# Performance work log

Hardware: AMD Instinct MI355X
Metric: run time of the kernel (lower is better)

The kernel has to match this reference:

```python
import jax, jax.numpy as jnp
import numpy as np

DEPTH_VALID_MIN = 1e-4   # cfg.depth_valid_min
IOU_THRESH = 0.02        # cfg.collision_iou_thresh
TOPK = 64                # cfg.collision_topk


def setup_inputs() -> dict:
    key = jax.random.key(0)
    k1, k2, k3, k4 = jax.random.split(key, 4)
    N, H, W = 128, 512, 512
    boxes = jax.random.uniform(k1, (N, 4), dtype=jnp.float32)
    masks = jax.random.uniform(k2, (N, H, W), dtype=jnp.float32)
    conf = jax.random.uniform(k3, (N,), dtype=jnp.float32)
    depth = jax.random.uniform(k4, (H, W), dtype=jnp.float32)
    return {"boxes": boxes, "masks": masks, "conf": conf, "depth": depth}


def _mask_depth_var(depth, mask):
    # population variance of depth pixels where mask>0.5 and depth>valid_min
    valid = (mask > 0.5) & (depth > DEPTH_VALID_MIN)
    cnt = jnp.sum(valid)
    cntf = jnp.maximum(cnt, 1).astype(depth.dtype)
    mean = jnp.sum(jnp.where(valid, depth, 0.0)) / cntf
    var = jnp.sum(jnp.where(valid, (depth - mean) ** 2, 0.0)) / cntf
    return jnp.where(cnt > 0, var, 0.0)


def reference(boxes, masks, conf, depth):
    N = boxes.shape[0]
    x1, y1, x2, y2 = boxes[:, 0], boxes[:, 1], boxes[:, 2], boxes[:, 3]
    bw = jnp.maximum(x2 - x1, 0.0)
    bh = jnp.maximum(y2 - y1, 0.0)
    area = jnp.clip(bw * bh, 0.0, 1.0)

    # per-detection masked depth variance (vectorized over N)
    d_var = jax.vmap(lambda m: _mask_depth_var(depth, m))(masks)  # [N]

    tall = jnp.clip(bh / (bw + 1e-6), 0.0, 10.0)
    thinness = jax.nn.sigmoid((tall - 1.2) * 2.0)
    unstable = jnp.clip(0.35 * thinness + 0.35 * jax.nn.sigmoid(d_var * 6.0)
                        + 0.3 * (1.0 - conf), 0.0, 1.0)
    slip = jnp.clip(0.45 * jax.nn.sigmoid(d_var * 8.0) + 0.25 * (1.0 - conf)
                    + 0.3 * jax.nn.sigmoid((area - 0.05) * 3.0), 0.0, 1.0)
    support = jnp.clip(1.0 - unstable, 0.0, 1.0)

    # pairwise IoU [N,N]
    xx1 = jnp.maximum(x1[:, None], x1[None, :])
    yy1 = jnp.maximum(y1[:, None], y1[None, :])
    xx2 = jnp.minimum(x2[:, None], x2[None, :])
    yy2 = jnp.minimum(y2[:, None], y2[None, :])
    inter = jnp.maximum(xx2 - xx1, 0.0) * jnp.maximum(yy2 - yy1, 0.0)
    a = bw * bh
    union = a[:, None] + a[None, :] - inter
    iou = inter / (union + 1e-6)
    iou = iou * (1.0 - jnp.eye(N, dtype=iou.dtype))  # fill_diagonal_(0)

    # collision pairs: top-k over off-diagonal IoUs above threshold (padded to TOPK)
    flat = iou.ravel()
    masked = jnp.where(flat > IOU_THRESH, flat, -1.0)
    vals, idx = jax.lax.top_k(masked, TOPK)
    valid = vals > IOU_THRESH
    pairs = jnp.where(valid[:, None],
                      jnp.stack([idx // N, idx % N], axis=-1), 0).astype(jnp.int32)
    collision = jnp.where(valid, jnp.clip(vals * 5.0, 0.0, 1.0), 0.0)

    return unstable, slip, support, pairs, collision
```

## Files before the change

### kernel.cpp

```cpp
#include <hip/hip_runtime.h>
#include <stdint.h>

#define N_BOX 128
#define HW    262144
#define SPLIT 16
#define CHUNK (HW / SPLIT)
#define TOPK  64
typedef unsigned long long u64;

__global__ __launch_bounds__(256) void k_mask_partial(
    const float* __restrict__ masks, const float* __restrict__ depth,
    float* __restrict__ part) {
  const int b = blockIdx.x;
  const int m = b >> 4;
  const int s = b & (SPLIT - 1);
  const float4* mk = reinterpret_cast<const float4*>(masks + (size_t)m * HW + (size_t)s * CHUNK);
  const float4* dp = reinterpret_cast<const float4*>(depth + (size_t)s * CHUNK);
  const int t = threadIdx.x;

  float c = 0.f, s1 = 0.f, s2 = 0.f;
#pragma unroll
  for (int j = 0; j < 16; ++j) {
    const int i = t + j * 256;
    float4 mv = mk[i];
    float4 dv = dp[i];
    if (mv.x > 0.5f && dv.x > 1e-4f) { c += 1.f; s1 += dv.x; s2 += dv.x * dv.x; }
    if (mv.y > 0.5f && dv.y > 1e-4f) { c += 1.f; s1 += dv.y; s2 += dv.y * dv.y; }
    if (mv.z > 0.5f && dv.z > 1e-4f) { c += 1.f; s1 += dv.z; s2 += dv.z * dv.z; }
    if (mv.w > 0.5f && dv.w > 1e-4f) { c += 1.f; s1 += dv.w; s2 += dv.w * dv.w; }
  }
  for (int off = 32; off > 0; off >>= 1) {
    c  += __shfl_down(c,  off);
    s1 += __shfl_down(s1, off);
    s2 += __shfl_down(s2, off);
  }
  __shared__ float red[3][4];
  const int wid = t >> 6, lane = t & 63;
  if (lane == 0) { red[0][wid] = c; red[1][wid] = s1; red[2][wid] = s2; }
  __syncthreads();
  if (t == 0) {
    part[b * 3 + 0] = red[0][0] + red[0][1] + red[0][2] + red[0][3];
    part[b * 3 + 1] = red[1][0] + red[1][1] + red[1][2] + red[1][3];
    part[b * 3 + 2] = red[2][0] + red[2][1] + red[2][2] + red[2][3];
  }
}

__device__ __forceinline__ u64 sort64_desc(u64 v, int lane) {
#pragma unroll
  for (int size = 2; size <= 64; size <<= 1) {
#pragma unroll
    for (int stride = size >> 1; stride > 0; stride >>= 1) {
      const u64 o = __shfl_xor(v, stride);
      const bool blk   = ((lane & size) == 0);
      const bool lower = ((lane & stride) == 0);
      const u64 mx = (v > o) ? v : o;
      const u64 mn = (v > o) ? o : v;
      v = (blk == lower) ? mx : mn;
    }
  }
  return v;
}

__device__ __forceinline__ u64 merge64_desc(u64 v, u64 s, int lane) {
  const u64 r = __shfl_xor(s, 63);
  v = (v > r) ? v : r;
#pragma unroll
  for (int stride = 32; stride > 0; stride >>= 1) {
    const u64 o = __shfl_xor(v, stride);
    const bool lower = ((lane & stride) == 0);
    const u64 mx = (v > o) ? v : o;
    const u64 mn = (v > o) ? o : v;
    v = lower ? mx : mn;
  }
  return v;
}

__device__ __forceinline__ float sigf(float x) { return 1.f / (1.f + expf(-x)); }

__global__ __launch_bounds__(1024) void k_topk_fin(
    const float* __restrict__ boxes, const float* __restrict__ conf,
    const float* __restrict__ part, float* __restrict__ out) {
  __shared__ float X1[N_BOX], Y1[N_BOX], X2[N_BOX], Y2[N_BOX], A[N_BOX];
  __shared__ u64 wtop[16][TOPK];

  const int t = threadIdx.x;
  const int lane = t & 63;
  const int w = t >> 6;

  if (t < N_BOX) {
    const float x1 = boxes[t * 4 + 0], y1 = boxes[t * 4 + 1];
    const float x2 = boxes[t * 4 + 2], y2 = boxes[t * 4 + 3];
    X1[t] = x1; Y1[t] = y1; X2[t] = x2; Y2[t] = y2;
    A[t] = fmaxf(x2 - x1, 0.f) * fmaxf(y2 - y1, 0.f);
  }
  __syncthreads();

  u64 v = 0ULL;
#pragma unroll
  for (int b = 0; b < 16; ++b) {
    const int e = w * 1024 + b * 64 + lane;
    const int i = e >> 7, jj = e & 127;
    const float xx1 = fmaxf(X1[i], X1[jj]);
    const float yy1 = fmaxf(Y1[i], Y1[jj]);
    const float xx2 = fminf(X2[i], X2[jj]);
    const float yy2 = fminf(Y2[i], Y2[jj]);
    const float inter = fmaxf(xx2 - xx1, 0.f) * fmaxf(yy2 - yy1, 0.f);
    const float uni = A[i] + A[jj] - inter;
    float iou = inter / (uni + 1e-6f);
    if (i == jj) iou = 0.f;
    const float mval = (iou > 0.02f) ? iou : -1.0f;
    uint32_t u = __float_as_uint(mval);
    u = (u & 0x80000000u) ? ~u : (u | 0x80000000u);
    const u64 key = ((u64)u << 32) | (u64)(0xFFFFFFFFu - (uint32_t)e);

    if (b == 0) {
      v = sort64_desc(key, lane);
    } else {
      const u64 cut = __shfl(v, 63);
      if (__any(key > cut)) {
        const u64 s = sort64_desc(key, lane);
        v = merge64_desc(v, s, lane);
      }
    }
  }
  wtop[w][lane] = v;
  __syncthreads();

  if (w == 0) {
#pragma unroll
    for (int ww = 1; ww < 16; ++ww)
      v = merge64_desc(v, wtop[ww][lane], lane);
    const uint32_t mh = (uint32_t)(v >> 32);
    const uint32_t u  = (mh & 0x80000000u) ? (mh ^ 0x80000000u) : ~mh;
    const float val   = __uint_as_float(u);
    const uint32_t e  = 0xFFFFFFFFu - (uint32_t)(v & 0xFFFFFFFFu);
    const bool valid  = (val > 0.02f);
    out[3 * N_BOX + 2 * lane + 0] = valid ? (float)(e >> 7)  : 0.f;
    out[3 * N_BOX + 2 * lane + 1] = valid ? (float)(e & 127) : 0.f;
    out[3 * N_BOX + 2 * TOPK + lane] = valid ? fminf(fmaxf(val * 5.f, 0.f), 1.f) : 0.f;
  } else if (w == 2 || w == 3) {
    const int m = t - 128;
    float C = 0.f, S1 = 0.f, S2 = 0.f;
#pragma unroll
    for (int s = 0; s < SPLIT; ++s) {
      C  += part[(m * SPLIT + s) * 3 + 0];
      S1 += part[(m * SPLIT + s) * 3 + 1];
      S2 += part[(m * SPLIT + s) * 3 + 2];
    }
    const float cntf = fmaxf(C, 1.f);
    const float mean = S1 / cntf;
    float var = S2 / cntf - mean * mean;
    var = (C > 0.f) ? fmaxf(var, 0.f) : 0.f;

    const float x1 = X1[m], y1 = Y1[m], x2 = X2[m], y2 = Y2[m];
    const float bw = fmaxf(x2 - x1, 0.f);
    const float bh = fmaxf(y2 - y1, 0.f);
    const float area = fminf(fmaxf(bw * bh, 0.f), 1.f);
    const float cf = conf[m];
    const float tall = fminf(fmaxf(bh / (bw + 1e-6f), 0.f), 10.f);
    const float thin = sigf((tall - 1.2f) * 2.f);
    const float unst = fminf(fmaxf(0.35f * thin + 0.35f * sigf(var * 6.f) + 0.3f * (1.f - cf), 0.f), 1.f);
    const float slip = fminf(fmaxf(0.45f * sigf(var * 8.f) + 0.25f * (1.f - cf) + 0.3f * sigf((area - 0.05f) * 3.f), 0.f), 1.f);
    out[m]             = unst;
    out[N_BOX + m]     = slip;
    out[2 * N_BOX + m] = fminf(fmaxf(1.f - unst, 0.f), 1.f);
  }
}

extern "C" void kernel_launch(void* const* d_in, const int* in_sizes, int n_in,
                              void* d_out, int out_size, void* d_ws, size_t ws_size,
                              hipStream_t stream) {
  const float* boxes = (const float*)d_in[0];
  const float* masks = (const float*)d_in[1];
  const float* conf  = (const float*)d_in[2];
  const float* depth = (const float*)d_in[3];
  float* out  = (float*)d_out;
  float* part = (float*)d_ws;

  hipLaunchKernelGGL(k_mask_partial, dim3(N_BOX * SPLIT), dim3(256), 0, stream,
                     masks, depth, part);
  hipLaunchKernelGGL(k_topk_fin, dim3(1), dim3(1024), 0, stream,
                     boxes, conf, part, out);
}
```

Measured before the change: 218.3 us.

## Fuse mask reduction and top-k into one kernel with last-block finalize

```diff
diff --git a/kernel.cpp b/kernel.cpp
--- a/kernel.cpp
+++ b/kernel.cpp
@@ -6,44 +6,9 @@
 #define SPLIT 16
 #define CHUNK (HW / SPLIT)
 #define TOPK  64
+#define NMASKBLK (N_BOX * SPLIT)
 typedef unsigned long long u64;
-
-__global__ __launch_bounds__(256) void k_mask_partial(
-    const float* __restrict__ masks, const float* __restrict__ depth,
-    float* __restrict__ part) {
-  const int b = blockIdx.x;
-  const int m = b >> 4;
-  const int s = b & (SPLIT - 1);
-  const float4* mk = reinterpret_cast<const float4*>(masks + (size_t)m * HW + (size_t)s * CHUNK);
-  const float4* dp = reinterpret_cast<const float4*>(depth + (size_t)s * CHUNK);
-  const int t = threadIdx.x;
-
-  float c = 0.f, s1 = 0.f, s2 = 0.f;
-#pragma unroll
-  for (int j = 0; j < 16; ++j) {
-    const int i = t + j * 256;
-    float4 mv = mk[i];
-    float4 dv = dp[i];
-    if (mv.x > 0.5f && dv.x > 1e-4f) { c += 1.f; s1 += dv.x; s2 += dv.x * dv.x; }
-    if (mv.y > 0.5f && dv.y > 1e-4f) { c += 1.f; s1 += dv.y; s2 += dv.y * dv.y; }
-    if (mv.z > 0.5f && dv.z > 1e-4f) { c += 1.f; s1 += dv.z; s2 += dv.z * dv.z; }
-    if (mv.w > 0.5f && dv.w > 1e-4f) { c += 1.f; s1 += dv.w; s2 += dv.w * dv.w; }
-  }
-  for (int off = 32; off > 0; off >>= 1) {
-    c  += __shfl_down(c,  off);
-    s1 += __shfl_down(s1, off);
-    s2 += __shfl_down(s2, off);
-  }
-  __shared__ float red[3][4];
-  const int wid = t >> 6, lane = t & 63;
-  if (lane == 0) { red[0][wid] = c; red[1][wid] = s1; red[2][wid] = s2; }
-  __syncthreads();
-  if (t == 0) {
-    part[b * 3 + 0] = red[0][0] + red[0][1] + red[0][2] + red[0][3];
-    part[b * 3 + 1] = red[1][0] + red[1][1] + red[1][2] + red[1][3];
-    part[b * 3 + 2] = red[2][0] + red[2][1] + red[2][2] + red[2][3];
-  }
-}
+typedef float vf4 __attribute__((ext_vector_type(4)));
 
 __device__ __forceinline__ u64 sort64_desc(u64 v, int lane) {
 #pragma unroll
@@ -77,93 +42,141 @@
 
 __device__ __forceinline__ float sigf(float x) { return 1.f / (1.f + expf(-x)); }
 
-__global__ __launch_bounds__(1024) void k_topk_fin(
-    const float* __restrict__ boxes, const float* __restrict__ conf,
-    const float* __restrict__ part, float* __restrict__ out) {
-  __shared__ float X1[N_BOX], Y1[N_BOX], X2[N_BOX], Y2[N_BOX], A[N_BOX];
-  __shared__ u64 wtop[16][TOPK];
-
+__global__ __launch_bounds__(1024) void k_fused(
+    const float* __restrict__ boxes, const float* __restrict__ masks,
+    const float* __restrict__ conf, const float* __restrict__ depth,
+    float* __restrict__ part, unsigned* __restrict__ cnt,
+    float* __restrict__ out) {
   const int t = threadIdx.x;
   const int lane = t & 63;
   const int w = t >> 6;
 
-  if (t < N_BOX) {
-    const float x1 = boxes[t * 4 + 0], y1 = boxes[t * 4 + 1];
-    const float x2 = boxes[t * 4 + 2], y2 = boxes[t * 4 + 3];
-    X1[t] = x1; Y1[t] = y1; X2[t] = x2; Y2[t] = y2;
-    A[t] = fmaxf(x2 - x1, 0.f) * fmaxf(y2 - y1, 0.f);
-  }
-  __syncthreads();
+  __shared__ float red[3][16];
+  __shared__ int   isLast;
+  __shared__ float X1[N_BOX], Y1[N_BOX], X2[N_BOX], Y2[N_BOX], A[N_BOX];
+  __shared__ u64   wtop[16][TOPK];
 
-  u64 v = 0ULL;
+  if (blockIdx.x < NMASKBLK) {
+    const int b = blockIdx.x;
+    const int m = b >> 4;
+    const int s = b & (SPLIT - 1);
+    const vf4* mk = reinterpret_cast<const vf4*>(masks + (size_t)m * HW + (size_t)s * CHUNK);
+    const vf4* dp = reinterpret_cast<const vf4*>(depth + (size_t)s * CHUNK);
+
+    float c = 0.f, s1 = 0.f, s2 = 0.f;
 #pragma unroll
-  for (int b = 0; b < 16; ++b) {
-    const int e = w * 1024 + b * 64 + lane;
-    const int i = e >> 7, jj = e & 127;
-    const float xx1 = fmaxf(X1[i], X1[jj]);
-    const float yy1 = fmaxf(Y1[i], Y1[jj]);
-    const float xx2 = fminf(X2[i], X2[jj]);
-    const float yy2 = fminf(Y2[i], Y2[jj]);
-    const float inter = fmaxf(xx2 - xx1, 0.f) * fmaxf(yy2 - yy1, 0.f);
-    const float uni = A[i] + A[jj] - inter;
-    float iou = inter / (uni + 1e-6f);
-    if (i == jj) iou = 0.f;
-    const float mval = (iou > 0.02f) ? iou : -1.0f;
-    uint32_t u = __float_as_uint(mval);
-    u = (u & 0x80000000u) ? ~u : (u | 0x80000000u);
-    const u64 key = ((u64)u << 32) | (u64)(0xFFFFFFFFu - (uint32_t)e);
+    for (int j = 0; j < 4; ++j) {
+      const int i = t + j * 1024;
+      const vf4 mv = __builtin_nontemporal_load(&mk[i]);
+      const vf4 dv = dp[i];
+      if (mv.x > 0.5f && dv.x > 1e-4f) { c += 1.f; s1 += dv.x; s2 += dv.x * dv.x; }
+      if (mv.y > 0.5f && dv.y > 1e-4f) { c += 1.f; s1 += dv.y; s2 += dv.y * dv.y; }
+      if (mv.z > 0.5f && dv.z > 1e-4f) { c += 1.f; s1 += dv.z; s2 += dv.z * dv.z; }
+      if (mv.w > 0.5f && dv.w > 1e-4f) { c += 1.f; s1 += dv.w; s2 += dv.w * dv.w; }
+    }
+    for (int off = 32; off > 0; off >>= 1) {
+      c  += __shfl_down(c,  off);
+      s1 += __shfl_down(s1, off);
+      s2 += __shfl_down(s2, off);
+    }
+    if (lane == 0) { red[0][w] = c; red[1][w] = s1; red[2][w] = s2; }
+    __syncthreads();
+    if (t == 0) {
+      float C = 0.f, S1 = 0.f, S2 = 0.f;
+#pragma unroll
+      for (int k = 0; k < 16; ++k) { C += red[0][k]; S1 += red[1][k]; S2 += red[2][k]; }
+      part[b * 3 + 0] = C;
+      part[b * 3 + 1] = S1;
+      part[b * 3 + 2] = S2;
+      __threadfence();
+      const unsigned tk = atomicAdd(cnt, 1u);
+      isLast = (tk == NMASKBLK - 1) ? 1 : 0;
+    }
+    __syncthreads();
 
-    if (b == 0) {
-      v = sort64_desc(key, lane);
-    } else {
-      const u64 cut = __shfl(v, 63);
-      if (__any(key > cut)) {
-        const u64 s = sort64_desc(key, lane);
-        v = merge64_desc(v, s, lane);
+    if (isLast && t < N_BOX) {
+      __threadfence();
+      volatile const float* vp = part;
+      const int m2 = t;
+      float C = 0.f, S1 = 0.f, S2 = 0.f;
+#pragma unroll
+      for (int s2i = 0; s2i < SPLIT; ++s2i) {
+        C  += vp[(m2 * SPLIT + s2i) * 3 + 0];
+        S1 += vp[(m2 * SPLIT + s2i) * 3 + 1];
+        S2 += vp[(m2 * SPLIT + s2i) * 3 + 2];
+      }
+      const float cntf = fmaxf(C, 1.f);
+      const float mean = S1 / cntf;
+      float var = S2 / cntf - mean * mean;
+      var = (C > 0.f) ? fmaxf(var, 0.f) : 0.f;
+
+      const float x1 = boxes[m2 * 4 + 0], y1 = boxes[m2 * 4 + 1];
+      const float x2 = boxes[m2 * 4 + 2], y2 = boxes[m2 * 4 + 3];
+      const float bw = fmaxf(x2 - x1, 0.f);
+      const float bh = fmaxf(y2 - y1, 0.f);
+      const float area = fminf(fmaxf(bw * bh, 0.f), 1.f);
+      const float cf = conf[m2];
+      const float tall = fminf(fmaxf(bh / (bw + 1e-6f), 0.f), 10.f);
+      const float thin = sigf((tall - 1.2f) * 2.f);
+      const float unst = fminf(fmaxf(0.35f * thin + 0.35f * sigf(var * 6.f) + 0.3f * (1.f - cf), 0.f), 1.f);
+      const float slip = fminf(fmaxf(0.45f * sigf(var * 8.f) + 0.25f * (1.f - cf) + 0.3f * sigf((area - 0.05f) * 3.f), 0.f), 1.f);
+      out[m2]             = unst;
+      out[N_BOX + m2]     = slip;
+      out[2 * N_BOX + m2] = fminf(fmaxf(1.f - unst, 0.f), 1.f);
+    }
+  } else {
+    if (t < N_BOX) {
+      const float x1 = boxes[t * 4 + 0], y1 = boxes[t * 4 + 1];
+      const float x2 = boxes[t * 4 + 2], y2 = boxes[t * 4 + 3];
+      X1[t] = x1; Y1[t] = y1; X2[t] = x2; Y2[t] = y2;
+      A[t] = fmaxf(x2 - x1, 0.f) * fmaxf(y2 - y1, 0.f);
+    }
+    __syncthreads();
+
+    u64 v = 0ULL;
+#pragma unroll
+    for (int b = 0; b < 16; ++b) {
+      const int e = w * 1024 + b * 64 + lane;
+      const int i = e >> 7, jj = e & 127;
+      const float xx1 = fmaxf(X1[i], X1[jj]);
+      const float yy1 = fmaxf(Y1[i], Y1[jj]);
+      const float xx2 = fminf(X2[i], X2[jj]);
+      const float yy2 = fminf(Y2[i], Y2[jj]);
+      const float inter = fmaxf(xx2 - xx1, 0.f) * fmaxf(yy2 - yy1, 0.f);
+      const float uni = A[i] + A[jj] - inter;
+      float iou = inter / (uni + 1e-6f);
+      if (i == jj) iou = 0.f;
+      const float mval = (iou > 0.02f) ? iou : -1.0f;
+      uint32_t u = __float_as_uint(mval);
+      u = (u & 0x80000000u) ? ~u : (u | 0x80000000u);
+      const u64 key = ((u64)u << 32) | (u64)(0xFFFFFFFFu - (uint32_t)e);
+
+      if (b == 0) {
+        v = sort64_desc(key, lane);
+      } else {
+        const u64 cut = __shfl(v, 63);
+        if (__any(key > cut)) {
+          const u64 s = sort64_desc(key, lane);
+          v = merge64_desc(v, s, lane);
+        }
       }
     }
-  }
-  wtop[w][lane] = v;
-  __syncthreads();
+    wtop[w][lane] = v;
+    __syncthreads();
 
-  if (w == 0) {
+    if (w == 0) {
 #pragma unroll
-    for (int ww = 1; ww < 16; ++ww)
-      v = merge64_desc(v, wtop[ww][lane], lane);
-    const uint32_t mh = (uint32_t)(v >> 32);
-    const uint32_t u  = (mh & 0x80000000u) ? (mh ^ 0x80000000u) : ~mh;
-    const float val   = __uint_as_float(u);
-    const uint32_t e  = 0xFFFFFFFFu - (uint32_t)(v & 0xFFFFFFFFu);
-    const bool valid  = (val > 0.02f);
-    out[3 * N_BOX + 2 * lane + 0] = valid ? (float)(e >> 7)  : 0.f;
-    out[3 * N_BOX + 2 * lane + 1] = valid ? (float)(e & 127) : 0.f;
-    out[3 * N_BOX + 2 * TOPK + lane] = valid ? fminf(fmaxf(val * 5.f, 0.f), 1.f) : 0.f;
-  } else if (w == 2 || w == 3) {
-    const int m = t - 128;
-    float C = 0.f, S1 = 0.f, S2 = 0.f;
-#pragma unroll
-    for (int s = 0; s < SPLIT; ++s) {
-      C  += part[(m * SPLIT + s) * 3 + 0];
-      S1 += part[(m * SPLIT + s) * 3 + 1];
-      S2 += part[(m * SPLIT + s) * 3 + 2];
+      for (int ww = 1; ww < 16; ++ww)
+        v = merge64_desc(v, wtop[ww][lane], lane);
+      const uint32_t mh = (uint32_t)(v >> 32);
+      const uint32_t u  = (mh & 0x80000000u) ? (mh ^ 0x80000000u) : ~mh;
+      const float val   = __uint_as_float(u);
+      const uint32_t e  = 0xFFFFFFFFu - (uint32_t)(v & 0xFFFFFFFFu);
+      const bool valid  = (val > 0.02f);
+      out[3 * N_BOX + 2 * lane + 0] = valid ? (float)(e >> 7)  : 0.f;
+      out[3 * N_BOX + 2 * lane + 1] = valid ? (float)(e & 127) : 0.f;
+      out[3 * N_BOX + 2 * TOPK + lane] = valid ? fminf(fmaxf(val * 5.f, 0.f), 1.f) : 0.f;
     }
-    const float cntf = fmaxf(C, 1.f);
-    const float mean = S1 / cntf;
-    float var = S2 / cntf - mean * mean;
-    var = (C > 0.f) ? fmaxf(var, 0.f) : 0.f;
-
-    const float x1 = X1[m], y1 = Y1[m], x2 = X2[m], y2 = Y2[m];
-    const float bw = fmaxf(x2 - x1, 0.f);
-    const float bh = fmaxf(y2 - y1, 0.f);
-    const float area = fminf(fmaxf(bw * bh, 0.f), 1.f);
-    const float cf = conf[m];
-    const float tall = fminf(fmaxf(bh / (bw + 1e-6f), 0.f), 10.f);
-    const float thin = sigf((tall - 1.2f) * 2.f);
-    const float unst = fminf(fmaxf(0.35f * thin + 0.35f * sigf(var * 6.f) + 0.3f * (1.f - cf), 0.f), 1.f);
-    const float slip = fminf(fmaxf(0.45f * sigf(var * 8.f) + 0.25f * (1.f - cf) + 0.3f * sigf((area - 0.05f) * 3.f), 0.f), 1.f);
-    out[m]             = unst;
-    out[N_BOX + m]     = slip;
-    out[2 * N_BOX + m] = fminf(fmaxf(1.f - unst, 0.f), 1.f);
   }
 }
 
@@ -176,9 +189,9 @@
   const float* depth = (const float*)d_in[3];
   float* out  = (float*)d_out;
   float* part = (float*)d_ws;
+  unsigned* cnt = (unsigned*)((char*)d_ws + 24576);
 
-  hipLaunchKernelGGL(k_mask_partial, dim3(N_BOX * SPLIT), dim3(256), 0, stream,
-                     masks, depth, part);
-  hipLaunchKernelGGL(k_topk_fin, dim3(1), dim3(1024), 0, stream,
-                     boxes, conf, part, out);
+  (void)hipMemsetAsync(cnt, 0, 4, stream);
+  hipLaunchKernelGGL(k_fused, dim3(NMASKBLK + 1), dim3(1024), 0, stream,
+                     boxes, masks, conf, depth, part, cnt, out);
 }
```

New measurement: 295.8 us. 1.35x slower.

## Buffer IoU candidates per wave and merge wave top-k lists as a tree

Applied to the files above, without the earlier changes.

```diff
diff --git a/kernel.cpp b/kernel.cpp
--- a/kernel.cpp
+++ b/kernel.cpp
@@ -82,6 +82,7 @@
     const float* __restrict__ part, float* __restrict__ out) {
   __shared__ float X1[N_BOX], Y1[N_BOX], X2[N_BOX], Y2[N_BOX], A[N_BOX];
   __shared__ u64 wtop[16][TOPK];
+  __shared__ u64 wcand[16][TOPK];
 
   const int t = threadIdx.x;
   const int lane = t & 63;
@@ -95,7 +96,8 @@
   }
   __syncthreads();
 
-  u64 v = 0ULL;
+  u64 run = 0ULL;
+  int nbuf = 0;
 #pragma unroll
   for (int b = 0; b < 16; ++b) {
     const int e = w * 1024 + b * 64 + lane;
@@ -108,28 +110,43 @@
     const float uni = A[i] + A[jj] - inter;
     float iou = inter / (uni + 1e-6f);
     if (i == jj) iou = 0.f;
-    const float mval = (iou > 0.02f) ? iou : -1.0f;
+    const bool cand = (iou > 0.02f);
+    const float mval = cand ? iou : -1.0f;
     uint32_t u = __float_as_uint(mval);
     u = (u & 0x80000000u) ? ~u : (u | 0x80000000u);
     const u64 key = ((u64)u << 32) | (u64)(0xFFFFFFFFu - (uint32_t)e);
 
     if (b == 0) {
-      v = sort64_desc(key, lane);
+      run = sort64_desc(key, lane);
     } else {
-      const u64 cut = __shfl(v, 63);
-      if (__any(key > cut)) {
-        const u64 s = sort64_desc(key, lane);
-        v = merge64_desc(v, s, lane);
+      const u64 mask = __ballot(cand);
+      const int nc = __popcll(mask);
+      if ((w == 0 && b == 1) || (nbuf + nc > TOPK)) {
+        run = merge64_desc(run, sort64_desc(key, lane), lane);
+      } else if (nc) {
+        const int pos = nbuf + __popcll(mask & ((1ULL << lane) - 1ULL));
+        if (cand) wcand[w][pos] = key;
+        nbuf += nc;
       }
     }
   }
-  wtop[w][lane] = v;
+  if (nbuf > 0) {
+    const u64 k = (lane < nbuf) ? wcand[w][lane] : 0ULL;
+    run = merge64_desc(run, sort64_desc(k, lane), lane);
+  }
+  wtop[w][lane] = run;
   __syncthreads();
 
+  for (int n = 8; n >= 1; n >>= 1) {
+    u64 a = 0ULL, bb = 0ULL;
+    if (w < n) { a = wtop[2 * w][lane]; bb = wtop[2 * w + 1][lane]; }
+    __syncthreads();
+    if (w < n) wtop[w][lane] = merge64_desc(a, bb, lane);
+    __syncthreads();
+  }
+
   if (w == 0) {
-#pragma unroll
-    for (int ww = 1; ww < 16; ++ww)
-      v = merge64_desc(v, wtop[ww][lane], lane);
+    const u64 v = wtop[0][lane];
     const uint32_t mh = (uint32_t)(v >> 32);
     const uint32_t u  = (mh & 0x80000000u) ? (mh ^ 0x80000000u) : ~mh;
     const float val   = __uint_as_float(u);
```

After: 209.5 us. 4.0% less time.
